# Performance work log

Measured on AMD Instinct MI355X. Metric: run time of the kernel, lower is better.

## Reference

```python
import jax, jax.numpy as jnp
import numpy as np
from jax import lax

NUM_NODES = 100000
FEAT = 256
RANK = 16
NNZ = 4000000
NUM_HE = 125000  # num_hyperedges == num_edges_total
K = 2000000      # int(0.5 * NNZ)


def setup_inputs() -> dict:
    key = jax.random.key(0)
    ks = jax.random.split(key, 6)
    x = jax.random.normal(ks[0], (NUM_NODES, FEAT), dtype=jnp.float32)
    W = jax.random.normal(ks[1], (RANK, FEAT), dtype=jnp.float32)
    edge_factors = jax.random.normal(ks[2], (NUM_HE, RANK), dtype=jnp.float32)
    V_idx = jax.random.randint(ks[3], (NNZ,), 0, NUM_NODES, dtype=jnp.int32)
    E_idx = jax.random.randint(ks[4], (NNZ,), 0, NUM_HE, dtype=jnp.int32)
    edge_ids = jax.random.randint(ks[5], (NUM_HE,), 0, NUM_HE, dtype=jnp.int32)
    return {"x": x, "W": W, "edge_factors": edge_factors,
            "V_idx": V_idx, "E_idx": E_idx, "edge_ids": edge_ids, "k": K}


def _segment_mean(vals, seg_ids, num_segments):
    s = jax.ops.segment_sum(vals, seg_ids, num_segments=num_segments)
    c = jax.ops.segment_sum(jnp.ones_like(vals), seg_ids, num_segments=num_segments)
    return s / jnp.maximum(c, 1.0)


def reference(x, W, edge_factors, V_idx, E_idx, edge_ids, k):
    # node_proj(x): [N, rank]; gather per-incidence node and edge factors, dot product
    proj = x @ W.T                                  # [N, rank]
    ef = edge_factors[edge_ids[E_idx]]              # [nnz, rank]
    logits = jnp.sum(proj[V_idx] * ef, axis=-1)     # [nnz]
    scores = jax.nn.sigmoid(logits)

    # is_test=True path: deterministic top-k keep set
    _, keep_ids = lax.top_k(scores, k)
    hard = jnp.zeros_like(scores).at[keep_ids].set(1.0)
    # straight-through: forward == hard, gradient flows through scores where hard==1
    soft = hard + (scores - lax.stop_gradient(scores)) * hard

    edge_probs = _segment_mean(lax.stop_gradient(scores), E_idx, NUM_HE)
    edge_soft = _segment_mean(soft, E_idx, NUM_HE)
    edge_hard = (_segment_mean(hard, E_idx, NUM_HE) > 0).astype(jnp.float32)
    return scores, soft, hard, edge_probs, edge_soft, edge_hard
```

## Files before the change

kernel.cpp:

```cpp
#include <hip/hip_runtime.h>
#include <math.h>

#define FEAT 256
#define RANKK 16
#define PRJ_NODES 16
#define CAND_CAP 131072
#define TIE_CAP 2048
#define NBK_MAX 512
#define PB_CHUNK 8192
#define SPLIT 4

typedef unsigned long long u64;

static __device__ __forceinline__ u64 pack_pair(unsigned e_low, unsigned bits, unsigned idx) {
    return ((u64)e_low << 56) | ((u64)bits << 26) | (u64)idx;
}

static __device__ __forceinline__ u64 pack_v(unsigned v, unsigned idx, unsigned e_low) {
    return ((u64)v << 40) | ((u64)idx << 8) | (u64)e_low;
}

__global__ __launch_bounds__(256) void ehist_scan(const int* __restrict__ E_idx,
        unsigned* __restrict__ bucketCnt, unsigned* __restrict__ bucketBase,
        unsigned* __restrict__ cursor, unsigned* __restrict__ ticket, int nnz) {
    __shared__ unsigned h[NBK_MAX];
    __shared__ unsigned ps[256];
    __shared__ unsigned isLast;
    int t = threadIdx.x;
    for (int j = t; j < NBK_MAX; j += 256) h[j] = 0;
    __syncthreads();
    for (int i = blockIdx.x * 256 + t; i < nnz; i += gridDim.x * 256)
        atomicAdd(&h[((unsigned)E_idx[i]) >> 8], 1u);
    __syncthreads();
    for (int j = t; j < NBK_MAX; j += 256)
        if (h[j]) atomicAdd(&bucketCnt[j], h[j]);
    __threadfence();
    if (t == 0) isLast = (atomicAdd(ticket, 1u) == gridDim.x - 1) ? 1u : 0u;
    __syncthreads();
    if (!isLast) return;
    unsigned a0 = atomicAdd(&bucketCnt[2 * t], 0u);
    unsigned a1 = atomicAdd(&bucketCnt[2 * t + 1], 0u);
    unsigned pairsum = a0 + a1;
    ps[t] = pairsum;
    __syncthreads();
    for (int off = 1; off < 256; off <<= 1) {
        unsigned v = (t >= off) ? ps[t - off] : 0u;
        __syncthreads();
        ps[t] += v;
        __syncthreads();
    }
    unsigned excl = ps[t] - pairsum;
    bucketBase[2 * t] = excl;           cursor[2 * t] = excl;
    bucketBase[2 * t + 1] = excl + a0;  cursor[2 * t + 1] = excl + a0;
    if (t == 255) bucketBase[NBK_MAX] = ps[255];
}

__global__ __launch_bounds__(256) void prep_combo(
        const float4* __restrict__ ef, const int* __restrict__ edge_ids,
        float4* __restrict__ ef2, int nhe,
        const float* __restrict__ x, const float* __restrict__ Wm,
        float* __restrict__ proj, int n_nodes, int G) {
    __shared__ float Ws[RANKK][FEAT + 4];
    __shared__ float Xs[PRJ_NODES][FEAT + 4];
    if ((int)blockIdx.x < G) {
        int t = blockIdx.x * 256 + threadIdx.x;
        if (t < nhe * 4) {
            int e = t >> 2, c = t & 3;
            ef2[(size_t)e * 4 + c] = ef[(size_t)edge_ids[e] * 4 + c];
        }
        return;
    }
    int pb = blockIdx.x - G;
    const float4* x4 = (const float4*)x;
    const float4* w4 = (const float4*)Wm;
    for (int t = threadIdx.x; t < RANKK * (FEAT / 4); t += 256) {
        int r = t >> 6, j4 = t & 63;
        *(float4*)&Ws[r][j4 * 4] = w4[t];
    }
    int nodeBase = pb * PRJ_NODES;
    for (int t = threadIdx.x; t < PRJ_NODES * (FEAT / 4); t += 256) {
        int n = t >> 6, j4 = t & 63;
        int node = nodeBase + n;
        float4 v = make_float4(0.f, 0.f, 0.f, 0.f);
        if (node < n_nodes) v = x4[(size_t)node * (FEAT / 4) + j4];
        *(float4*)&Xs[n][j4 * 4] = v;
    }
    __syncthreads();
    int n = threadIdx.x >> 4, r = threadIdx.x & 15;
    int node = nodeBase + n;
    if (node >= n_nodes) return;
    double acc = 0.0;
    #pragma unroll 8
    for (int j4 = 0; j4 < FEAT / 4; ++j4) {
        float4 xv = *(const float4*)&Xs[n][j4 * 4];
        float4 wv = *(const float4*)&Ws[r][j4 * 4];
        acc += (double)xv.x * (double)wv.x + (double)xv.y * (double)wv.y
             + (double)xv.z * (double)wv.z + (double)xv.w * (double)wv.w;
    }
    proj[(size_t)node * RANKK + r] = (float)acc;
}

__global__ __launch_bounds__(256) void sort_kernel(const int* __restrict__ V_idx,
        const int* __restrict__ E_idx, u64* __restrict__ vlist,
        unsigned* __restrict__ cursor, int nnz, int nb) {
    __shared__ unsigned bh[NBK_MAX];
    int t = threadIdx.x;
    for (int j = t; j < NBK_MAX; j += 256) bh[j] = 0;
    __syncthreads();
    int base = blockIdx.x * PB_CHUNK;
    int nE = nnz - base;
    if (nE > PB_CHUNK) nE = PB_CHUNK;
    for (int o = t; o < nE; o += 256)
        atomicAdd(&bh[((unsigned)E_idx[base + o]) >> 8], 1u);
    __syncthreads();
    for (int b = t; b < nb; b += 256) {
        unsigned c = bh[b];
        bh[b] = c ? atomicAdd(&cursor[b], c) : 0u;
    }
    __syncthreads();
    for (int o = t; o < nE; o += 256) {
        int i = base + o;
        unsigned e = (unsigned)E_idx[i];
        unsigned v = (unsigned)V_idx[i];
        unsigned pos = atomicAdd(&bh[e >> 8], 1u);
        vlist[pos] = pack_v(v, (unsigned)i, e & 255u);
    }
}

__global__ __launch_bounds__(256) void bucket_score(
        const float4* __restrict__ proj4, const float4* __restrict__ ef4,
        const unsigned* __restrict__ bucketBase, u64* __restrict__ list,
        float* __restrict__ scores, int nhe) {
    __shared__ float efs[256][20];
    int t = threadIdx.x;
    int b = blockIdx.x >> 2;
    int part = blockIdx.x & (SPLIT - 1);
    for (int jj = t; jj < 1024; jj += 256) {
        int edge = (b << 8) + (jj >> 2);
        if (edge < nhe) {
            float4 v = ef4[(size_t)edge * 4 + (jj & 3)];
            *(float4*)&efs[jj >> 2][(jj & 3) * 4] = v;
        }
    }
    __syncthreads();
    unsigned n0 = bucketBase[b], n1 = bucketBase[b + 1];
    #pragma unroll 2
    for (unsigned j = n0 + (part << 8) + t; j < n1; j += SPLIT * 256) {
        u64 p = list[j];
        unsigned v   = (unsigned)(p >> 40);
        unsigned idx = (unsigned)(p >> 8) & 0xFFFFFFu;
        unsigned el  = (unsigned)(p & 255u);
        float4 p0 = proj4[(size_t)v * 4 + 0];
        float4 p1 = proj4[(size_t)v * 4 + 1];
        float4 p2 = proj4[(size_t)v * 4 + 2];
        float4 p3 = proj4[(size_t)v * 4 + 3];
        float4 f0 = *(const float4*)&efs[el][0];
        float4 f1 = *(const float4*)&efs[el][4];
        float4 f2 = *(const float4*)&efs[el][8];
        float4 f3 = *(const float4*)&efs[el][12];
        double acc = (double)p0.x * f0.x + (double)p0.y * f0.y + (double)p0.z * f0.z + (double)p0.w * f0.w
                   + (double)p1.x * f1.x + (double)p1.y * f1.y + (double)p1.z * f1.z + (double)p1.w * f1.w
                   + (double)p2.x * f2.x + (double)p2.y * f2.y + (double)p2.z * f2.z + (double)p2.w * f2.w
                   + (double)p3.x * f3.x + (double)p3.y * f3.y + (double)p3.z * f3.z + (double)p3.w * f3.w;
        float s = (float)(1.0 / (1.0 + exp(-acc)));
        scores[idx] = s;
        list[j] = pack_pair(el, __float_as_uint(s), idx);
    }
}

__global__ __launch_bounds__(256) void score_linear(
        const float4* __restrict__ proj4, const float4* __restrict__ ef4,
        const int* __restrict__ V_idx, const int* __restrict__ E_idx,
        float* __restrict__ scores, int nnz) {
    int stride = gridDim.x * blockDim.x;
    #pragma unroll 2
    for (int i = blockIdx.x * blockDim.x + threadIdx.x; i < nnz; i += stride) {
        int v = V_idx[i], e = E_idx[i];
        float4 p0 = proj4[(size_t)v * 4 + 0];
        float4 p1 = proj4[(size_t)v * 4 + 1];
        float4 p2 = proj4[(size_t)v * 4 + 2];
        float4 p3 = proj4[(size_t)v * 4 + 3];
        float4 f0 = ef4[(size_t)e * 4 + 0];
        float4 f1 = ef4[(size_t)e * 4 + 1];
        float4 f2 = ef4[(size_t)e * 4 + 2];
        float4 f3 = ef4[(size_t)e * 4 + 3];
        double acc = (double)p0.x * f0.x + (double)p0.y * f0.y + (double)p0.z * f0.z + (double)p0.w * f0.w
                   + (double)p1.x * f1.x + (double)p1.y * f1.y + (double)p1.z * f1.z + (double)p1.w * f1.w
                   + (double)p2.x * f2.x + (double)p2.y * f2.y + (double)p2.z * f2.z + (double)p2.w * f2.w
                   + (double)p3.x * f3.x + (double)p3.y * f3.y + (double)p3.z * f3.z + (double)p3.w * f3.w;
        scores[i] = (float)(1.0 / (1.0 + exp(-acc)));
    }
}

__global__ __launch_bounds__(256) void pair_build(const int* __restrict__ E_idx,
        const float* __restrict__ scores, u64* __restrict__ pairs,
        unsigned* __restrict__ cursor, int nnz, int nb) {
    __shared__ unsigned bh[NBK_MAX];
    for (int t = threadIdx.x; t < NBK_MAX; t += 256) bh[t] = 0;
    __syncthreads();
    int base = blockIdx.x * PB_CHUNK;
    int nE = nnz - base;
    if (nE > PB_CHUNK) nE = PB_CHUNK;
    for (int o = threadIdx.x; o < nE; o += 256)
        atomicAdd(&bh[((unsigned)E_idx[base + o]) >> 8], 1u);
    __syncthreads();
    for (int b = threadIdx.x; b < nb; b += 256) {
        unsigned c = bh[b];
        bh[b] = c ? atomicAdd(&cursor[b], c) : 0u;
    }
    __syncthreads();
    for (int o = threadIdx.x; o < nE; o += 256) {
        int i = base + o;
        unsigned e = (unsigned)E_idx[i];
        unsigned bits = __float_as_uint(scores[i]);
        unsigned pos = atomicAdd(&bh[e >> 8], 1u);
        pairs[pos] = pack_pair(e & 255u, bits, (unsigned)i);
    }
}

__global__ void hist1_kernel(const float4* __restrict__ scores4, unsigned* __restrict__ hist1g,
                             int n4, int nnz) {
    __shared__ unsigned h[4096];
    for (int t = threadIdx.x; t < 4096; t += blockDim.x) h[t] = 0;
    __syncthreads();
    unsigned r1016 = 0, r1015 = 0, r0 = 0;
    int stride = gridDim.x * blockDim.x;
    for (int i = blockIdx.x * blockDim.x + threadIdx.x; i < n4; i += stride) {
        float4 sv = scores4[i];
        unsigned bb[4] = {__float_as_uint(sv.x), __float_as_uint(sv.y),
                          __float_as_uint(sv.z), __float_as_uint(sv.w)};
        #pragma unroll
        for (int q = 0; q < 4; ++q) {
            unsigned b = bb[q] >> 20;
            if (b == 1016) ++r1016;
            else if (b == 1015) ++r1015;
            else if (b == 0) ++r0;
            else atomicAdd(&h[b], 1u);
        }
    }
    for (int i = n4 * 4 + blockIdx.x * blockDim.x + threadIdx.x; i < nnz; i += stride) {
        unsigned b = __float_as_uint(((const float*)scores4)[i]) >> 20;
        if (b == 1016) ++r1016;
        else if (b == 1015) ++r1015;
        else if (b == 0) ++r0;
        else atomicAdd(&h[b], 1u);
    }
    if (r1016) atomicAdd(&h[1016], r1016);
    if (r1015) atomicAdd(&h[1015], r1015);
    if (r0) atomicAdd(&h[0], r0);
    __syncthreads();
    for (int t = threadIdx.x; t < 4096; t += blockDim.x)
        if (h[t]) atomicAdd(&hist1g[t], h[t]);
}

__global__ void scan1_kernel(const unsigned* __restrict__ hist,
                             unsigned* __restrict__ sel, const int* __restrict__ kptr) {
    __shared__ unsigned sfx[256];
    int t = threadIdx.x;
    unsigned local[16];
    unsigned s = 0;
    #pragma unroll
    for (int j = 0; j < 16; ++j) { local[j] = hist[t * 16 + j]; s += local[j]; }
    sfx[t] = s;
    __syncthreads();
    for (int off = 1; off < 256; off <<= 1) {
        unsigned add = (t + off < 256) ? sfx[t + off] : 0;
        __syncthreads();
        sfx[t] += add;
        __syncthreads();
    }
    unsigned krem = (unsigned)(*kptr);
    unsigned above = (t + 1 < 256) ? sfx[t + 1] : 0;
    if (above < krem && sfx[t] >= krem) {
        unsigned cum = above;
        int b = t * 16;
        for (int j = 15; j >= 0; --j) {
            unsigned cc = local[j];
            if (cum + cc >= krem) { b = t * 16 + j; break; }
            cum += cc;
        }
        sel[0] = krem - cum;
        sel[1] = ((unsigned)b) << 20;
    }
}

__global__ void compact_kernel(const float4* __restrict__ scores4,
                               const unsigned* __restrict__ sel,
                               uint2* __restrict__ cand, unsigned* __restrict__ candCount,
                               int n4, int nnz) {
    unsigned pref = sel[1] >> 20;
    int tid = blockIdx.x * blockDim.x + threadIdx.x;
    int stride = gridDim.x * blockDim.x;
    int lane = threadIdx.x & 63;
    int niter = (n4 + stride - 1) / stride;
    for (int kk = 0; kk < niter; ++kk) {
        int i = tid + kk * stride;
        bool inb = (i < n4);
        float4 sv = make_float4(0.f, 0.f, 0.f, 0.f);
        if (inb) sv = scores4[i];
        unsigned bb[4] = {__float_as_uint(sv.x), __float_as_uint(sv.y),
                          __float_as_uint(sv.z), __float_as_uint(sv.w)};
        #pragma unroll
        for (int q = 0; q < 4; ++q) {
            bool pred = inb && ((bb[q] >> 20) == pref);
            unsigned long long mask = __ballot(pred);
            if (mask) {
                int leader = __ffsll(mask) - 1;
                unsigned base = 0;
                if (lane == leader) base = atomicAdd(candCount, (unsigned)__popcll(mask));
                base = __shfl(base, leader, 64);
                if (pred) {
                    unsigned rank = __popcll(mask & ((1ull << lane) - 1ull));
                    unsigned pos = base + rank;
                    if (pos < CAND_CAP) cand[pos] = make_uint2(bb[q], (unsigned)(i * 4 + q));
                }
            }
        }
    }
    for (int i = n4 * 4 + tid; i < nnz; i += stride) {
        unsigned b = __float_as_uint(((const float*)scores4)[i]);
        if ((b >> 20) == pref) {
            unsigned pos = atomicAdd(candCount, 1u);
            if (pos < CAND_CAP) cand[pos] = make_uint2(b, (unsigned)i);
        }
    }
}

__global__ __launch_bounds__(256) void select_small(const uint2* __restrict__ cand,
                            const unsigned* __restrict__ candCount,
                            unsigned* __restrict__ sel, unsigned* __restrict__ tieList) {
    __shared__ unsigned h2[4096];
    __shared__ unsigned sfx[256];
    __shared__ unsigned sB2, sKrem2, sT, sM;
    __shared__ unsigned h3[256];
    __shared__ unsigned ties[TIE_CAP];
    __shared__ unsigned tcnt;
    int t = threadIdx.x;
    unsigned nc = *candCount;
    int n = (nc < CAND_CAP) ? (int)nc : CAND_CAP;
    unsigned krem = sel[0];
    unsigned pref = sel[1];

    for (int j = t; j < 4096; j += 256) h2[j] = 0;
    if (t == 0) tcnt = 0;
    __syncthreads();
    for (int j = t; j < n; j += 256) atomicAdd(&h2[(cand[j].x >> 8) & 0xFFF], 1u);
    __syncthreads();

    unsigned local[16];
    unsigned s = 0;
    #pragma unroll
    for (int j = 0; j < 16; ++j) { local[j] = h2[t * 16 + j]; s += local[j]; }
    sfx[t] = s;
    __syncthreads();
    for (int off = 1; off < 256; off <<= 1) {
        unsigned add = (t + off < 256) ? sfx[t + off] : 0;
        __syncthreads();
        sfx[t] += add;
        __syncthreads();
    }
    {
        unsigned above = (t + 1 < 256) ? sfx[t + 1] : 0;
        if (above < krem && sfx[t] >= krem) {
            unsigned cum = above;
            int b = t * 16;
            for (int j = 15; j >= 0; --j) {
                unsigned cc = local[j];
                if (cum + cc >= krem) { b = t * 16 + j; break; }
                cum += cc;
            }
            sB2 = (unsigned)b;
            sKrem2 = krem - cum;
        }
    }
    __syncthreads();

    h3[t] = 0;
    __syncthreads();
    unsigned b2 = sB2;
    for (int j = t; j < n; j += 256) {
        unsigned x = cand[j].x;
        if (((x >> 8) & 0xFFF) == b2) atomicAdd(&h3[x & 0xFF], 1u);
    }
    __syncthreads();
    sfx[t] = h3[t];
    __syncthreads();
    for (int off = 1; off < 256; off <<= 1) {
        unsigned add = (t + off < 256) ? sfx[t + off] : 0;
        __syncthreads();
        sfx[t] += add;
        __syncthreads();
    }
    {
        unsigned krem2 = sKrem2;
        unsigned above = (t + 1 < 256) ? sfx[t + 1] : 0;
        if (above < krem2 && sfx[t] >= krem2) {
            sT = pref | (b2 << 8) | (unsigned)t;
            sM = krem2 - above;
        }
    }
    __syncthreads();

    unsigned T = sT;
    for (int j = t; j < n; j += 256) {
        if (cand[j].x == T) {
            unsigned p = atomicAdd(&tcnt, 1u);
            if (p < TIE_CAP) ties[p] = cand[j].y;
        }
    }
    __syncthreads();
    if (t == 0) {
        unsigned cnt = (tcnt < TIE_CAP) ? tcnt : TIE_CAP;
        for (unsigned a = 1; a < cnt; ++a) {
            unsigned key = ties[a];
            int bpos = (int)a - 1;
            while (bpos >= 0 && ties[bpos] > key) { ties[bpos + 1] = ties[bpos]; --bpos; }
            ties[bpos + 1] = key;
        }
        unsigned m = sM;
        if (m > cnt) m = cnt;
        sel[2] = T;
        sel[3] = m;
        for (unsigned j = 0; j < m; ++j) tieList[j] = ties[j];
    }
}

__global__ __launch_bounds__(256) void edge_final(const u64* __restrict__ pairs,
        const unsigned* __restrict__ bucketBase, const unsigned* __restrict__ sel,
        const unsigned* __restrict__ tieList,
        float* __restrict__ eprob, float* __restrict__ esoft, float* __restrict__ ehard,
        int nhe) {
    __shared__ float ss[256];
    __shared__ unsigned cc[256];
    __shared__ unsigned hh[256];
    __shared__ unsigned ties[TIE_CAP];
    unsigned T = sel[2];
    unsigned m = sel[3];
    if (m > TIE_CAP) m = TIE_CAP;
    int t = threadIdx.x;
    ss[t] = 0.f; cc[t] = 0u; hh[t] = 0u;
    for (int j = t; j < (int)m; j += 256) ties[j] = tieList[j];
    __syncthreads();
    int b = blockIdx.x;
    unsigned n0 = bucketBase[b], n1 = bucketBase[b + 1];
    for (unsigned j = n0 + t; j < n1; j += 256) {
        u64 p = pairs[j];
        unsigned el = (unsigned)(p >> 56);
        unsigned bits = (unsigned)(p >> 26) & 0x3FFFFFFFu;
        atomicAdd(&ss[el], __uint_as_float(bits));
        atomicAdd(&cc[el], 1u);
        bool keep = bits > T;
        if (bits == T) {
            unsigned idx = (unsigned)(p & 0x3FFFFFFu);
            int lo = 0, hi = (int)m - 1;
            keep = false;
            while (lo <= hi) {
                int mid = (lo + hi) >> 1;
                unsigned v = ties[mid];
                if (v == idx) { keep = true; break; }
                if (v < idx) lo = mid + 1; else hi = mid - 1;
            }
        }
        if (keep) atomicAdd(&hh[el], 1u);
    }
    __syncthreads();
    int e = b * 256 + t;
    if (e < nhe) {
        float c = fmaxf((float)cc[t], 1.0f);
        eprob[e] = ss[t] / c;
        esoft[e] = (float)hh[t] / c;
        ehard[e] = (hh[t] > 0) ? 1.0f : 0.0f;
    }
}

__global__ __launch_bounds__(256) void write_hard(const float4* __restrict__ scores4,
                           const unsigned* __restrict__ sel,
                           const unsigned* __restrict__ tieList,
                           float4* __restrict__ hard4, float4* __restrict__ soft4,
                           int n4, int nnz) {
    __shared__ unsigned ties[TIE_CAP];
    unsigned T = sel[2];
    unsigned m = sel[3];
    if (m > TIE_CAP) m = TIE_CAP;
    for (int j = threadIdx.x; j < (int)m; j += blockDim.x) ties[j] = tieList[j];
    __syncthreads();
    int tid = blockIdx.x * blockDim.x + threadIdx.x;
    int stride = gridDim.x * blockDim.x;
    for (int i = tid; i < n4; i += stride) {
        float4 sv = scores4[i];
        unsigned bb[4] = {__float_as_uint(sv.x), __float_as_uint(sv.y),
                          __float_as_uint(sv.z), __float_as_uint(sv.w)};
        float hv[4];
        #pragma unroll
        for (int q = 0; q < 4; ++q) {
            bool keep = (bb[q] > T);
            if (bb[q] == T) {
                unsigned idx = (unsigned)(i * 4 + q);
                int lo = 0, hi = (int)m - 1;
                keep = false;
                while (lo <= hi) {
                    int mid = (lo + hi) >> 1;
                    unsigned v = ties[mid];
                    if (v == idx) { keep = true; break; }
                    if (v < idx) lo = mid + 1; else hi = mid - 1;
                }
            }
            hv[q] = keep ? 1.0f : 0.0f;
        }
        float4 outv = make_float4(hv[0], hv[1], hv[2], hv[3]);
        hard4[i] = outv;
        soft4[i] = outv;
    }
    const float* sc = (const float*)scores4;
    float* hard = (float*)hard4;
    float* soft = (float*)soft4;
    for (int i = n4 * 4 + tid; i < nnz; i += stride) {
        unsigned b = __float_as_uint(sc[i]);
        bool keep = (b > T);
        if (b == T) {
            unsigned idx = (unsigned)i;
            int lo = 0, hi = (int)m - 1;
            keep = false;
            while (lo <= hi) {
                int mid = (lo + hi) >> 1;
                unsigned v = ties[mid];
                if (v == idx) { keep = true; break; }
                if (v < idx) lo = mid + 1; else hi = mid - 1;
            }
        }
        float hvv = keep ? 1.0f : 0.0f;
        hard[i] = hvv;
        soft[i] = hvv;
    }
}

extern "C" void kernel_launch(void* const* d_in, const int* in_sizes, int n_in,
                              void* d_out, int out_size, void* d_ws, size_t ws_size,
                              hipStream_t stream) {
    const float* x        = (const float*)d_in[0];
    const float* Wm       = (const float*)d_in[1];
    const float* ef       = (const float*)d_in[2];
    const int*   V_idx    = (const int*)d_in[3];
    const int*   E_idx    = (const int*)d_in[4];
    const int*   edge_ids = (const int*)d_in[5];
    const int*   kptr     = (const int*)d_in[6];

    const int nnz     = in_sizes[3];
    const int nhe     = in_sizes[5];
    const int n_nodes = in_sizes[0] / FEAT;
    const int nb      = (nhe + 255) >> 8;

    float* out    = (float*)d_out;
    float* scores = out;
    float* soft   = out + (size_t)nnz;
    float* hard   = out + 2 * (size_t)nnz;
    float* eprob  = out + 3 * (size_t)nnz;
    float* esoft  = eprob + nhe;
    float* ehard  = esoft + nhe;

    u64*   vlist = (u64*)soft;
    uint2* cand  = (uint2*)eprob;

    char* w = (char*)d_ws;
    unsigned* hist1      = (unsigned*)w;
    unsigned* bucketCnt  = hist1 + 4096;
    unsigned* candCount  = bucketCnt + NBK_MAX;
    unsigned* ticket1    = candCount + 1;
    unsigned* sel        = ticket1 + 1;
    unsigned* tieList    = sel + 8;
    unsigned* bucketBase = tieList + TIE_CAP;
    unsigned* cursor     = bucketBase + NBK_MAX + 1;
    char* auxEnd = (char*)(cursor + NBK_MAX);
    size_t auxAligned = (((size_t)(auxEnd - w)) + 255) & ~(size_t)255;
    size_t zeroBytes = (size_t)(4096 + NBK_MAX + 2) * sizeof(unsigned);

    size_t ef2Bytes  = (size_t)nhe * RANKK * sizeof(float);
    size_t projBytes = (size_t)n_nodes * RANKK * sizeof(float);

    bool wsBig = (ws_size >= auxAligned + ef2Bytes + projBytes);
    float* ef2;
    float* proj;
    if (wsBig) {
        ef2  = (float*)(w + auxAligned);
        proj = (float*)(w + auxAligned + ef2Bytes);
    } else {
        ef2  = hard;
        proj = hard + (size_t)nhe * RANKK;
    }

    hipMemsetAsync(w, 0, zeroBytes, stream);

    ehist_scan<<<128, 256, 0, stream>>>(E_idx, bucketCnt, bucketBase, cursor, ticket1, nnz);

    int G = (nhe * 4 + 255) / 256;
    int P = (n_nodes + PRJ_NODES - 1) / PRJ_NODES;
    prep_combo<<<G + P, 256, 0, stream>>>((const float4*)ef, edge_ids, (float4*)ef2, nhe,
                                          x, Wm, proj, n_nodes, G);

    int nChunks = (nnz + PB_CHUNK - 1) / PB_CHUNK;
    if (wsBig) {
        sort_kernel<<<nChunks, 256, 0, stream>>>(V_idx, E_idx, vlist, cursor, nnz, nb);
        bucket_score<<<nb * SPLIT, 256, 0, stream>>>(
            (const float4*)proj, (const float4*)ef2, bucketBase, vlist, scores, nhe);
    } else {
        score_linear<<<2048, 256, 0, stream>>>(
            (const float4*)proj, (const float4*)ef2, V_idx, E_idx, scores, nnz);
        pair_build<<<nChunks, 256, 0, stream>>>(E_idx, scores, vlist, cursor, nnz, nb);
    }

    int n4 = nnz / 4;
    hist1_kernel<<<128, 256, 0, stream>>>((const float4*)scores, hist1, n4, nnz);
    scan1_kernel<<<1, 256, 0, stream>>>(hist1, sel, kptr);
    compact_kernel<<<1024, 256, 0, stream>>>(
        (const float4*)scores, sel, cand, candCount, n4, nnz);
    select_small<<<1, 256, 0, stream>>>(cand, candCount, sel, tieList);

    edge_final<<<nb, 256, 0, stream>>>(vlist, bucketBase, sel, tieList,
                                       eprob, esoft, ehard, nhe);
    write_hard<<<1024, 256, 0, stream>>>(
        (const float4*)scores, sel, tieList, (float4*)hard, (float4*)soft, n4, nnz);
}
```

Measured before the change: 475.0 us.

## Register-tile node projection 2x2 with larger node blocks and chunked features

Each block of the projection part of prep_combo now handles 64 nodes instead of 16. Each thread computes a 2-node by 2-rank tile of fp64 accumulators, and the 256-wide feature dimension is staged through shared memory in two 128-wide chunks. The aim is to reuse each shared-memory load across several FMAs, to load W into shared memory four times less often in total, and to launch fewer blocks. The cost is an extra sync round per chunk and four double accumulators per thread, with fewer blocks available to hide latency.

```diff
diff --git a/kernel.cpp b/kernel.cpp
--- a/kernel.cpp
+++ b/kernel.cpp
@@ -3,12 +3,12 @@
 
 #define FEAT 256
 #define RANKK 16
-#define PRJ_NODES 16
 #define CAND_CAP 131072
 #define TIE_CAP 2048
 #define NBK_MAX 512
 #define PB_CHUNK 8192
 #define SPLIT 4
+#define PRJ_NODES 64
 
 typedef unsigned long long u64;
 
@@ -61,7 +61,7 @@
         const float* __restrict__ x, const float* __restrict__ Wm,
         float* __restrict__ proj, int n_nodes, int G) {
     __shared__ float Ws[RANKK][FEAT + 4];
-    __shared__ float Xs[PRJ_NODES][FEAT + 4];
+    __shared__ float Xs[PRJ_NODES][128 + 4];
     if ((int)blockIdx.x < G) {
         int t = blockIdx.x * 256 + threadIdx.x;
         if (t < nhe * 4) {
@@ -73,31 +73,48 @@
     int pb = blockIdx.x - G;
     const float4* x4 = (const float4*)x;
     const float4* w4 = (const float4*)Wm;
-    for (int t = threadIdx.x; t < RANKK * (FEAT / 4); t += 256) {
-        int r = t >> 6, j4 = t & 63;
-        *(float4*)&Ws[r][j4 * 4] = w4[t];
+    for (int i = threadIdx.x; i < RANKK * 64; i += 256) {
+        int r = i >> 6, c4 = i & 63;
+        *(float4*)&Ws[r][c4 * 4] = w4[(size_t)r * 64 + c4];
     }
     int nodeBase = pb * PRJ_NODES;
-    for (int t = threadIdx.x; t < PRJ_NODES * (FEAT / 4); t += 256) {
-        int n = t >> 6, j4 = t & 63;
-        int node = nodeBase + n;
-        float4 v = make_float4(0.f, 0.f, 0.f, 0.f);
-        if (node < n_nodes) v = x4[(size_t)node * (FEAT / 4) + j4];
-        *(float4*)&Xs[n][j4 * 4] = v;
-    }
-    __syncthreads();
-    int n = threadIdx.x >> 4, r = threadIdx.x & 15;
-    int node = nodeBase + n;
-    if (node >= n_nodes) return;
-    double acc = 0.0;
-    #pragma unroll 8
-    for (int j4 = 0; j4 < FEAT / 4; ++j4) {
-        float4 xv = *(const float4*)&Xs[n][j4 * 4];
-        float4 wv = *(const float4*)&Ws[r][j4 * 4];
-        acc += (double)xv.x * (double)wv.x + (double)xv.y * (double)wv.y
-             + (double)xv.z * (double)wv.z + (double)xv.w * (double)wv.w;
-    }
-    proj[(size_t)node * RANKK + r] = (float)acc;
+    int np = threadIdx.x >> 3;
+    int rp = threadIdx.x & 7;
+    int n0 = np * 2, r0 = rp * 2;
+    double a00 = 0.0, a01 = 0.0, a10 = 0.0, a11 = 0.0;
+    for (int chunk = 0; chunk < 2; ++chunk) {
+        __syncthreads();
+        for (int i = threadIdx.x; i < PRJ_NODES * 32; i += 256) {
+            int row = i >> 5, c4 = i & 31;
+            int node = nodeBase + row;
+            float4 v = make_float4(0.f, 0.f, 0.f, 0.f);
+            if (node < n_nodes) v = x4[(size_t)node * 64 + chunk * 32 + c4];
+            *(float4*)&Xs[row][c4 * 4] = v;
+        }
+        __syncthreads();
+        int jw = chunk * 128;
+        #pragma unroll 8
+        for (int j4 = 0; j4 < 32; ++j4) {
+            float4 xa = *(const float4*)&Xs[n0][j4 * 4];
+            float4 xb = *(const float4*)&Xs[n0 + 1][j4 * 4];
+            float4 wa = *(const float4*)&Ws[r0][jw + j4 * 4];
+            float4 wb = *(const float4*)&Ws[r0 + 1][jw + j4 * 4];
+            a00 += (double)xa.x * wa.x + (double)xa.y * wa.y + (double)xa.z * wa.z + (double)xa.w * wa.w;
+            a01 += (double)xa.x * wb.x + (double)xa.y * wb.y + (double)xa.z * wb.z + (double)xa.w * wb.w;
+            a10 += (double)xb.x * wa.x + (double)xb.y * wa.y + (double)xb.z * wa.z + (double)xb.w * wa.w;
+            a11 += (double)xb.x * wb.x + (double)xb.y * wb.y + (double)xb.z * wb.z + (double)xb.w * wb.w;
+        }
+    }
+    int nodeA = nodeBase + n0;
+    int nodeB = nodeA + 1;
+    if (nodeA < n_nodes) {
+        proj[(size_t)nodeA * RANKK + r0]     = (float)a00;
+        proj[(size_t)nodeA * RANKK + r0 + 1] = (float)a01;
+    }
+    if (nodeB < n_nodes) {
+        proj[(size_t)nodeB * RANKK + r0]     = (float)a10;
+        proj[(size_t)nodeB * RANKK + r0 + 1] = (float)a11;
+    }
 }
 
 __global__ __launch_bounds__(256) void sort_kernel(const int* __restrict__ V_idx,
```

Result: no change. 472.6 us (-0.5%).
